# Kernel optimization log

Measured on AMD Instinct MI355X. Metric: run time of the kernel, lower is better.

The kernel has to match this reference:

```python
import jax, jax.numpy as jnp
import numpy as np

D = 256; H = 8; DH = D // H; FF = 1024; L = 2048; M = 1024


def _mlp(x, w0, b0, w1, b1, w2, b2):
    # 3-layer MLP, relu on all but last (matches MLP class)
    x = jax.nn.relu(x @ w0 + b0)
    x = jax.nn.relu(x @ w1 + b1)
    return x @ w2 + b2


def _ln(x, g, b, eps=1e-5):
    m = jnp.mean(x, axis=-1, keepdims=True)
    v = jnp.var(x, axis=-1, keepdims=True)
    return (x - m) * jax.lax.rsqrt(v + eps) * g + b


def setup_inputs():
    key = jax.random.key(0)
    ks = jax.random.split(key, 16)
    p = lambda i, shape: jax.random.normal(ks[i], shape, jnp.float32) * 0.02
    z = lambda *s: jnp.zeros(s, jnp.float32)
    o = lambda *s: jnp.ones(s, jnp.float32)
    # positions: ego covers [0, L), agent covers [L-M, 2L-M) -> exactly M shared positions
    return {
        'ego_q': jax.random.normal(ks[0], (1, L, D), jnp.float32),
        'agent_q': jax.random.normal(ks[1], (1, L, D), jnp.float32),
        'ego_pos': jnp.arange(L, dtype=jnp.int32),
        'agent_pos': jnp.arange(L, dtype=jnp.int32) + (L - M),
        'n_match': M,
        'fw0': p(2, (2 * D, D)), 'fb0': z(D),
        'fw1': p(3, (D, D)), 'fb1': z(D),
        'fw2': p(4, (D, D)), 'fb2': z(D),
        'wq': p(5, (D, D)), 'bq': z(D),
        'wk': p(6, (D, D)), 'bk': z(D),
        'wv': p(7, (D, D)), 'bv': z(D),
        'wo': p(8, (D, D)), 'bo': z(D),
        'g1': o(D), 'be1': z(D),
        'l1w': p(9, (D, FF)), 'l1b': z(FF),
        'l2w': p(10, (FF, D)), 'l2b': z(D),
        'g2': o(D), 'be2': z(D),
    }


def reference(ego_q, agent_q, ego_pos, agent_pos, n_match,
              fw0, fb0, fw1, fb1, fw2, fb2,
              wq, bq, wk, bk, wv, bv, wo, bo,
              g1, be1, l1w, l1b, l2w, l2b, g2, be2):
    La = agent_pos.shape[0]
    # vectorized replacement of the per-position dict/loop grouping:
    # for each ego position, find a matching agent position (positions sorted+unique)
    idx = jnp.clip(jnp.searchsorted(agent_pos, ego_pos), 0, La - 1)
    matched = (agent_pos[idx] == ego_pos)                     # (L,)
    pair = jnp.concatenate([ego_q, agent_q[:, idx, :]], axis=-1)  # (1, L, 2D)
    fused = _mlp(pair, fw0, fb0, fw1, fb1, fw2, fb2)          # (1, L, D)
    ego_out = jnp.where(matched[None, :, None], fused, ego_q)
    # agent queries whose positions are NOT in ego's set: indices [n_match, La)
    q = jnp.concatenate([ego_out, agent_q[:, n_match:, :]], axis=1)  # (1, 2L-M, D)
    kv = jnp.concatenate([ego_q, agent_q], axis=1)                   # (1, 2L, D)
    # MultiheadAttention (batch_first, eval mode -> no dropout)
    qh = (q @ wq + bq).reshape(1, -1, H, DH)
    kh = (kv @ wk + bk).reshape(1, -1, H, DH)
    vh = (kv @ wv + bv).reshape(1, -1, H, DH)
    scores = jnp.einsum('bqhd,bkhd->bhqk', qh, kh) * (1.0 / np.sqrt(DH))
    attn = jax.nn.softmax(scores, axis=-1)
    o = jnp.einsum('bhqk,bkhd->bqhd', attn, vh).reshape(1, -1, D) @ wo + bo
    x = _ln(q + o, g1, be1)
    ff = jax.nn.relu(x @ l1w + l1b) @ l2w + l2b
    return _ln(x + ff, g2, be2)
```

## Files before the change

### kernel.cpp

```cpp
#include <hip/hip_runtime.h>
#include <hip/hip_bf16.h>

typedef __hip_bfloat16 bf16;
typedef __bf16 bf16x8 __attribute__((ext_vector_type(8)));
typedef float  f32x16 __attribute__((ext_vector_type(16)));

__device__ __forceinline__ bool is_bf16_flag(const unsigned* g1w) {
    return *g1w == 0x3F803F80u;
}

__device__ __forceinline__ unsigned cvt_pk_bf16(float lo, float hi) {
    unsigned w;
    asm("v_cvt_pk_bf16_f32 %0, %1, %2" : "=v"(w) : "v"(lo), "v"(hi));
    return w;
}
__device__ __forceinline__ void permlane32_swap(unsigned& a, unsigned& b) {
    asm("v_permlane32_swap_b32 %0, %1" : "+v"(a), "+v"(b));
}

union FragU { unsigned u[4]; uint4 q; bf16x8 v; };

__device__ __forceinline__ float loadf(const void* p, size_t i, bool isb) {
    return isb ? __bfloat162float(((const bf16*)p)[i]) : ((const float*)p)[i];
}

__device__ __forceinline__ float4 load4rt(const void* p, size_t i, bool isb) {
    if (isb) {
        uint2 u = *(const uint2*)((const bf16*)p + i);
        float4 f;
        f.x = __uint_as_float(u.x << 16);
        f.y = __uint_as_float(u.x & 0xFFFF0000u);
        f.z = __uint_as_float(u.y << 16);
        f.w = __uint_as_float(u.y & 0xFFFF0000u);
        return f;
    }
    return *(const float4*)((const float*)p + i);
}

__device__ __forceinline__ void store4b(bf16* p, float4 v) {
    uint2 w;
    w.x = cvt_pk_bf16(v.x, v.y);
    w.y = cvt_pk_bf16(v.z, v.w);
    *(uint2*)p = w;
}

__device__ __forceinline__ float4 load4b(const bf16* p) {
    uint2 u = *(const uint2*)p;
    float4 f;
    f.x = __uint_as_float(u.x << 16);
    f.y = __uint_as_float(u.x & 0xFFFF0000u);
    f.z = __uint_as_float(u.y << 16);
    f.w = __uint_as_float(u.y & 0xFFFF0000u);
    return f;
}

#define NCVT 13
#define NWT 9
struct PreArgs {
    const void* csrc[NCVT];
    float*      cdst[NCVT];
    float       cscale[NCVT];
    int         cn4[NCVT];
    int         cblk_end[NCVT];
    int         cvt_blocks;
    const void* wsrc[NWT];
    bf16*       wdst[NWT];
    int         wK[NWT];
    int         wN[NWT];
    float       wscale[NWT];
    int         wblk_end[NWT];
    int         wt_blocks;
    const void* ego; const void* agent;
    const int*  epos; const int* apos;
    int         La; int L; int Mm;
    bf16*       pair;
    int*        mflag;
    int         pair_blocks;
    bf16*       kvb;
    int         kv_blocks;
    bf16*       qb;
};

__global__ void preprocess_kernel(PreArgs a, const unsigned* __restrict__ g1w) {
    bool isb = is_bf16_flag(g1w);
    __shared__ float ld[64][65];
    __shared__ int s_idx[2];
    int b = blockIdx.x;
    int tid = threadIdx.x;
    if (b < a.cvt_blocks) {
        int t = 0;
        while (b >= a.cblk_end[t]) t++;
        int base = (t == 0) ? 0 : a.cblk_end[t - 1];
        int i = (b - base) * 256 + tid;
        if (i >= a.cn4[t]) return;
        float sc = a.cscale[t];
        float4 r = load4rt(a.csrc[t], (size_t)i * 4, isb);
        r.x *= sc; r.y *= sc; r.z *= sc; r.w *= sc;
        ((float4*)a.cdst[t])[i] = r;
    } else if (b < a.cvt_blocks + a.wt_blocks) {
        b -= a.cvt_blocks;
        int w = 0;
        while (b >= a.wblk_end[w]) w++;
        int base = (w == 0) ? 0 : a.wblk_end[w - 1];
        int tt = b - base;
        int tn = a.wN[w] >> 6;
        int kr = (tt / tn) * 64, nc = (tt % tn) * 64;
        int N = a.wN[w], K = a.wK[w];
        float sc = a.wscale[w];
        const void* src = a.wsrc[w];
#pragma unroll
        for (int i = 0; i < 16; i++) {
            int f = tid + i * 256;
            int r = f >> 6, c = f & 63;
            ld[r][c] = loadf(src, (size_t)(kr + r) * N + nc + c, isb) * sc;
        }
        __syncthreads();
        bf16* dst = a.wdst[w];
#pragma unroll
        for (int i = 0; i < 16; i++) {
            int f = tid + i * 256;
            int c = f >> 6, r = f & 63;
            dst[(size_t)(nc + c) * K + kr + r] = __float2bfloat16(ld[r][c]);
        }
    } else if (b < a.cvt_blocks + a.wt_blocks + a.pair_blocks) {
        b -= a.cvt_blocks + a.wt_blocks;
        int rb = tid >> 7;
        int row = b * 2 + rb;
        int cc = (tid & 127) * 4;
        if ((tid & 127) == 0) {
            int p = a.epos[row];
            int lo = 0, hi = a.La;
            while (lo < hi) { int mid = (lo + hi) >> 1; if (a.apos[mid] < p) lo = mid + 1; else hi = mid; }
            int idx = lo < a.La - 1 ? lo : a.La - 1;
            s_idx[rb] = idx;
            a.mflag[row] = (a.apos[idx] == p) ? 1 : 0;
        }
        __syncthreads();
        int idx = s_idx[rb];
        float4 v = (cc < 256) ? load4rt(a.ego, (size_t)row * 256 + cc, isb)
                              : load4rt(a.agent, (size_t)idx * 256 + (cc - 256), isb);
        store4b(a.pair + (size_t)row * 512 + cc, v);
    } else if (b < a.cvt_blocks + a.wt_blocks + a.pair_blocks + a.kv_blocks) {
        b -= a.cvt_blocks + a.wt_blocks + a.pair_blocks;
        int wave = tid >> 6, lane = tid & 63;
        int r = b * 4 + wave;
        int col = lane * 4;
        float4 kvv = (r < a.L) ? load4rt(a.ego, (size_t)r * 256 + col, isb)
                               : load4rt(a.agent, (size_t)(r - a.L) * 256 + col, isb);
        store4b(a.kvb + (size_t)r * 256 + col, kvv);
    } else {
        b -= a.cvt_blocks + a.wt_blocks + a.pair_blocks + a.kv_blocks;
        int wave = tid >> 6, lane = tid & 63;
        int r = b * 4 + wave;
        int col = lane * 4;
        float4 qv = (r < a.L) ? load4rt(a.ego, (size_t)r * 256 + col, isb)
                              : load4rt(a.agent, (size_t)(a.Mm + r - a.L) * 256 + col, isb);
        store4b(a.qb + (size_t)r * 256 + col, qv);
    }
}

template<int RELU, int WMASK>
__device__ __forceinline__ void gemm_core(const bf16* __restrict__ A, const bf16* __restrict__ Bt,
                                          const float* __restrict__ bias, bf16* __restrict__ C,
                                          int K, int lda, int ldb, int ldc,
                                          int bm, int bn, bool addBias,
                                          const int* __restrict__ wmask,
                                          char* sA, char* sB) {
    const int t = threadIdx.x;
    const int lane = t & 63, wave = t >> 6;
    const int hi = lane >> 5, ql = lane & 31;
    const int wm = (wave & 1) * 32, wn = (wave >> 1) * 32;

    const int r0 = t >> 3, ch0 = t & 7;
    const int r1 = 32 + r0;
    const int wb0 = (r0 * 128 + ch0 * 16) ^ ((r0 & 7) << 4);
    const int wb1 = (r1 * 128 + ch0 * 16) ^ ((r1 & 7) << 4);

    uint4 ra0, ra1, rb0, rb1;
    ra0 = *(const uint4*)&A [(size_t)(bm + r0) * lda + ch0 * 8];
    ra1 = *(const uint4*)&A [(size_t)(bm + r1) * lda + ch0 * 8];
    rb0 = *(const uint4*)&Bt[(size_t)(bn + r0) * ldb + ch0 * 8];
    rb1 = *(const uint4*)&Bt[(size_t)(bn + r1) * ldb + ch0 * 8];

    f32x16 acc = {};
    const int swzA = ((wm + ql) & 7) << 4;
    const int swzB = ((wn + ql) & 7) << 4;
    const int rowA = (wm + ql) * 128;
    const int rowB = (wn + ql) * 128;

    for (int k0 = 0; k0 < K; k0 += 64) {
        __syncthreads();
        *(uint4*)(sA + wb0) = ra0;
        *(uint4*)(sA + wb1) = ra1;
        *(uint4*)(sB + wb0) = rb0;
        *(uint4*)(sB + wb1) = rb1;
        if (k0 + 64 < K) {
            int kn = k0 + 64;
            ra0 = *(const uint4*)&A [(size_t)(bm + r0) * lda + kn + ch0 * 8];
            ra1 = *(const uint4*)&A [(size_t)(bm + r1) * lda + kn + ch0 * 8];
            rb0 = *(const uint4*)&Bt[(size_t)(bn + r0) * ldb + kn + ch0 * 8];
            rb1 = *(const uint4*)&Bt[(size_t)(bn + r1) * ldb + kn + ch0 * 8];
        }
        __syncthreads();
#pragma unroll
        for (int kc = 0; kc < 4; kc++) {
            FragU af, bf_;
            af.q  = *(const uint4*)(sA + ((rowA + kc * 32 + hi * 16) ^ swzA));
            bf_.q = *(const uint4*)(sB + ((rowB + kc * 32 + hi * 16) ^ swzB));
            acc = __builtin_amdgcn_mfma_f32_32x32x16_bf16(af.v, bf_.v, acc, 0, 0, 0);
        }
    }

    int gn = bn + wn + ql;
    float bsv = addBias ? bias[gn] : 0.f;
#pragma unroll
    for (int r = 0; r < 16; r++) {
        int mrow = (r & 3) + 8 * (r >> 2) + 4 * hi;
        int grow = bm + wm + mrow;
        float v = acc[r] + bsv;
        if (RELU) v = fmaxf(v, 0.f);
        if (!WMASK || wmask[grow])
            C[(size_t)grow * ldc + gn] = __float2bfloat16(v);
    }
}

template<int RELU>
__launch_bounds__(256)
__global__ void gemm_bf16_kernel(const bf16* __restrict__ A, const bf16* __restrict__ Bt,
                                 const float* __restrict__ bias, bf16* __restrict__ C,
                                 int M, int N, int K, int lda, int ldb, int ldc) {
    __shared__ __align__(16) char sA[64 * 128];
    __shared__ __align__(16) char sB[64 * 128];
    const int z = blockIdx.z;
    gemm_core<RELU, 0>(A + (size_t)z * K, Bt + (size_t)z * K, bias, C + (size_t)z * M * ldc,
                       K, lda, ldb, ldc, blockIdx.y * 64, blockIdx.x * 64, z == 0, nullptr, sA, sB);
}

template<int RELU>
__launch_bounds__(256)
__global__ void gemm_masked_kernel(const bf16* __restrict__ A, const bf16* __restrict__ Bt,
                                   const float* __restrict__ bias, bf16* __restrict__ C,
                                   int K, int lda, int ldb, int ldc,
                                   const int* __restrict__ wmask) {
    __shared__ __align__(16) char sA[64 * 128];
    __shared__ __align__(16) char sB[64 * 128];
    gemm_core<RELU, 1>(A, Bt, bias, C, K, lda, ldb, ldc,
                       blockIdx.y * 64, blockIdx.x * 64, true, wmask, sA, sB);
}

struct GemmP {
    const bf16* A; const bf16* Bt; const float* bias; bf16* C;
    int K, lda, ldb, ldc, nx;
};

template<int R0, int R1>
__launch_bounds__(256)
__global__ void gemm_dual_kernel(GemmP p0, GemmP p1, int nblk0) {
    __shared__ __align__(16) char sA[64 * 128];
    __shared__ __align__(16) char sB[64 * 128];
    int b = blockIdx.x;
    if (b < nblk0) {
        int bn = (b % p0.nx) * 64, bm = (b / p0.nx) * 64;
        gemm_core<R0, 0>(p0.A, p0.Bt, p0.bias, p0.C, p0.K, p0.lda, p0.ldb, p0.ldc, bm, bn, true, nullptr, sA, sB);
    } else {
        b -= nblk0;
        int bn = (b % p1.nx) * 64, bm = (b / p1.nx) * 64;
        gemm_core<R1, 0>(p1.A, p1.Bt, p1.bias, p1.C, p1.K, p1.lda, p1.ldb, p1.ldc, bm, bn, true, nullptr, sA, sB);
    }
}

#define SPLITS 8

__launch_bounds__(256)
__global__ void attn_mfma_kernel(const bf16* __restrict__ qh,
                                 const bf16* __restrict__ kvh,
                                 float* __restrict__ pm, float* __restrict__ pl,
                                 bf16* __restrict__ pacc,
                                 int Nq, int Nk) {
    __shared__ __align__(16) char sK[2][64 * 128];
    __shared__ __align__(16) char sV[2][32 * 128];

    const int h = blockIdx.y, z = blockIdx.z;
    const int t = threadIdx.x;
    const int wave = t >> 6, lane = t & 63;
    const int ql = lane & 31, hi = lane >> 5;
    const int qbase = blockIdx.x * 128 + wave * 32;
    const int kbeg = z * (Nk / SPLITS);
    const int nkk = Nk / SPLITS;

    FragU qf0, qf1;
    {
        const bf16* qp = qh + (size_t)(qbase + ql) * 256 + h * 32;
        qf0.q = *(const uint4*)(qp + hi * 8);
        qf1.q = *(const uint4*)(qp + 16 + hi * 8);
    }

    float mrun = -1e30f, lrun = 0.f;
    f32x16 acc = {};

    const int skey = t >> 2, sch = t & 3;
    const int kwb = (skey * 128 + sch * 16) ^ ((skey & 7) << 4);

    uint4 rk = *(const uint4*)(kvh + (size_t)(kbeg + skey) * 512 + h * 32 + sch * 8);
    uint4 rv = *(const uint4*)(kvh + (size_t)(kbeg + lane) * 512 + 256 + h * 32 + wave * 8);

    int cur = 0;
#pragma unroll 1
    for (int t0 = 0; t0 < nkk; t0 += 64) {
        char* sKc = sK[cur];
        char* sVc = sV[cur];
        *(uint4*)(sKc + kwb) = rk;
        {
            unsigned short sv[8] = {
                (unsigned short)(rv.x), (unsigned short)(rv.x >> 16),
                (unsigned short)(rv.y), (unsigned short)(rv.y >> 16),
                (unsigned short)(rv.z), (unsigned short)(rv.z >> 16),
                (unsigned short)(rv.w), (unsigned short)(rv.w >> 16)};
#pragma unroll
            for (int i = 0; i < 8; i++) {
                int dh = wave * 8 + i;
                *(unsigned short*)(sVc + dh * 128 + ((lane * 2) ^ (i << 4))) = sv[i];
            }
        }
        if (t0 + 64 < nkk) {
            rk = *(const uint4*)(kvh + (size_t)(kbeg + t0 + 64 + skey) * 512 + h * 32 + sch * 8);
            rv = *(const uint4*)(kvh + (size_t)(kbeg + t0 + 64 + lane) * 512 + 256 + h * 32 + wave * 8);
        }
        __syncthreads();

        FragU ka, kb;
        f32x16 s0 = {}, s1 = {};
        {
            int row0 = ql, row1 = 32 + ql;
            int swzk = (ql & 7) << 4;
            ka.q = *(const uint4*)(sKc + ((row0 * 128 + hi * 16) ^ swzk));
            s0 = __builtin_amdgcn_mfma_f32_32x32x16_bf16(ka.v, qf0.v, s0, 0, 0, 0);
            ka.q = *(const uint4*)(sKc + ((row0 * 128 + 32 + hi * 16) ^ swzk));
            s0 = __builtin_amdgcn_mfma_f32_32x32x16_bf16(ka.v, qf1.v, s0, 0, 0, 0);
            kb.q = *(const uint4*)(sKc + ((row1 * 128 + hi * 16) ^ swzk));
            s1 = __builtin_amdgcn_mfma_f32_32x32x16_bf16(kb.v, qf0.v, s1, 0, 0, 0);
            kb.q = *(const uint4*)(sKc + ((row1 * 128 + 32 + hi * 16) ^ swzk));
            s1 = __builtin_amdgcn_mfma_f32_32x32x16_bf16(kb.v, qf1.v, s1, 0, 0, 0);
        }

        float tm = -1e30f;
#pragma unroll
        for (int r = 0; r < 16; r++) tm = fmaxf(tm, fmaxf(s0[r], s1[r]));
        tm = fmaxf(tm, __shfl_xor(tm, 32));
        if (!__all(tm <= mrun)) {
            float mn = fmaxf(mrun, tm);
            float cf = __builtin_amdgcn_exp2f(mrun - mn);
            mrun = mn;
#pragma unroll
            for (int r = 0; r < 16; r++) acc[r] *= cf;
            lrun *= cf;
        }

        float p0[16], p1[16];
        float ls = 0.f;
#pragma unroll
        for (int r = 0; r < 16; r++) { p0[r] = __builtin_amdgcn_exp2f(s0[r] - mrun); ls += p0[r]; }
#pragma unroll
        for (int r = 0; r < 16; r++) { p1[r] = __builtin_amdgcn_exp2f(s1[r] - mrun); ls += p1[r]; }
        ls += __shfl_xor(ls, 32);
        lrun += ls;

        int swzk = (ql & 7) << 4;
        FragU vf, pa;
        {
            unsigned a = cvt_pk_bf16(p0[0], p0[1]),  b = cvt_pk_bf16(p0[2], p0[3]);
            unsigned c = cvt_pk_bf16(p0[4], p0[5]),  d = cvt_pk_bf16(p0[6], p0[7]);
            permlane32_swap(a, c); permlane32_swap(b, d);
            pa.u[0] = a; pa.u[1] = b; pa.u[2] = c; pa.u[3] = d;
            vf.q = *(const uint4*)(sVc + ((ql * 128 + hi * 16) ^ swzk));
            acc = __builtin_amdgcn_mfma_f32_32x32x16_bf16(vf.v, pa.v, acc, 0, 0, 0);
            unsigned e = cvt_pk_bf16(p0[8], p0[9]),   f = cvt_pk_bf16(p0[10], p0[11]);
            unsigned g = cvt_pk_bf16(p0[12], p0[13]), h2 = cvt_pk_bf16(p0[14], p0[15]);
            permlane32_swap(e, g); permlane32_swap(f, h2);
            pa.u[0] = e; pa.u[1] = f; pa.u[2] = g; pa.u[3] = h2;
            vf.q = *(const uint4*)(sVc + ((ql * 128 + 32 + hi * 16) ^ swzk));
            acc = __builtin_amdgcn_mfma_f32_32x32x16_bf16(vf.v, pa.v, acc, 0, 0, 0);
        }
        {
            unsigned a = cvt_pk_bf16(p1[0], p1[1]),  b = cvt_pk_bf16(p1[2], p1[3]);
            unsigned c = cvt_pk_bf16(p1[4], p1[5]),  d = cvt_pk_bf16(p1[6], p1[7]);
            permlane32_swap(a, c); permlane32_swap(b, d);
            pa.u[0] = a; pa.u[1] = b; pa.u[2] = c; pa.u[3] = d;
            vf.q = *(const uint4*)(sVc + ((ql * 128 + 64 + hi * 16) ^ swzk));
            acc = __builtin_amdgcn_mfma_f32_32x32x16_bf16(vf.v, pa.v, acc, 0, 0, 0);
            unsigned e = cvt_pk_bf16(p1[8], p1[9]),   f = cvt_pk_bf16(p1[10], p1[11]);
            unsigned g = cvt_pk_bf16(p1[12], p1[13]), h2 = cvt_pk_bf16(p1[14], p1[15]);
            permlane32_swap(e, g); permlane32_swap(f, h2);
            pa.u[0] = e; pa.u[1] = f; pa.u[2] = g; pa.u[3] = h2;
            vf.q = *(const uint4*)(sVc + ((ql * 128 + 96 + hi * 16) ^ swzk));
            acc = __builtin_amdgcn_mfma_f32_32x32x16_bf16(vf.v, pa.v, acc, 0, 0, 0);
        }
        cur ^= 1;
    }

    if (hi == 0) {
        pm[((size_t)z * 8 + h) * Nq + qbase + ql] = mrun;
        pl[((size_t)z * 8 + h) * Nq + qbase + ql] = lrun;
    }
#pragma unroll
    for (int r = 0; r < 16; r++) {
        int dh = (r & 3) + 8 * (r >> 2) + 4 * hi;
        pacc[(((size_t)z * 8 + h) * 32 + dh) * (size_t)Nq + qbase + ql] = __float2bfloat16(acc[r]);
    }
}

__global__ void attn_merge_kernel(const float* __restrict__ pm, const float* __restrict__ pl,
                                  const bf16* __restrict__ pacc, bf16* __restrict__ o, int Nq) {
    int q = blockIdx.x * 256 + threadIdx.x;
    int h = blockIdx.y, dg = blockIdx.z;
    float ml[SPLITS];
    float M = -1e30f;
#pragma unroll
    for (int s = 0; s < SPLITS; s++) {
        ml[s] = pm[((size_t)s * 8 + h) * Nq + q];
        M = fmaxf(M, ml[s]);
    }
    float L = 0.f;
    float w[SPLITS];
#pragma unroll
    for (int s = 0; s < SPLITS; s++) {
        w[s] = __builtin_amdgcn_exp2f(ml[s] - M);
        L += pl[((size_t)s * 8 + h) * Nq + q] * w[s];
    }
    float inv = 1.f / L;
#pragma unroll
    for (int j = 0; j < 4; j++) {
        int d = dg * 4 + j;
        float a = 0.f;
#pragma unroll
        for (int s = 0; s < SPLITS; s++)
            a += __bfloat162float(pacc[(((size_t)s * 8 + h) * 32 + d) * (size_t)Nq + q]) * w[s];
        o[(size_t)q * 256 + h * 32 + d] = __float2bfloat16(a * inv);
    }
}

__global__ void ln_kernel(const bf16* __restrict__ a, const bf16* __restrict__ b,
                          const bf16* __restrict__ c,
                          const float* __restrict__ g, const float* __restrict__ be,
                          bf16* __restrict__ outf16, void* __restrict__ outb,
                          const unsigned* __restrict__ g1w) {
    int wave = threadIdx.x >> 6, lane = threadIdx.x & 63;
    int row = blockIdx.x * 4 + wave;
    int col = lane * 4;
    size_t base = (size_t)row * 256 + col;
    float4 av = load4b(a + base);
    float4 bv = load4b(b + base);
    float x0 = av.x + bv.x, x1 = av.y + bv.y, x2 = av.z + bv.z, x3 = av.w + bv.w;
    if (c) {
        float4 cv = load4b(c + base);
        x0 += cv.x; x1 += cv.y; x2 += cv.z; x3 += cv.w;
    }
    float s  = x0 + x1 + x2 + x3;
    float s2 = x0 * x0 + x1 * x1 + x2 * x2 + x3 * x3;
#pragma unroll
    for (int off = 32; off; off >>= 1) { s += __shfl_xor(s, off); s2 += __shfl_xor(s2, off); }
    float mean = s * (1.f / 256.f);
    float var  = s2 * (1.f / 256.f) - mean * mean;
    float rs = rsqrtf(var + 1e-5f);
    float4 gv = *(const float4*)(g + col);
    float4 bev = *(const float4*)(be + col);
    float y0 = (x0 - mean) * rs * gv.x + bev.x;
    float y1 = (x1 - mean) * rs * gv.y + bev.y;
    float y2 = (x2 - mean) * rs * gv.z + bev.z;
    float y3 = (x3 - mean) * rs * gv.w + bev.w;
    if (outf16) {
        store4b(outf16 + base, make_float4(y0, y1, y2, y3));
    } else if (is_bf16_flag(g1w)) {
        store4b((bf16*)outb + base, make_float4(y0, y1, y2, y3));
    } else {
        *(float4*)((float*)outb + base) = make_float4(y0, y1, y2, y3);
    }
}

extern "C" void kernel_launch(void* const* d_in, const int* in_sizes, int n_in,
                              void* d_out, int out_size, void* d_ws, size_t ws_size,
                              hipStream_t stream) {
    const int Dd = 256;
    const int L  = in_sizes[2];
    const int La = in_sizes[3];
    const int Nk = L + La;
    const int Nq = out_size / Dd;
    const int Mm = L + La - Nq;
    const float scale = 0.17677669529663687f * 1.4426950408889634f;

    const unsigned* g1w = (const unsigned*)d_in[19];

    float* W = (float*)d_ws;
    size_t off = 0;
    auto alloc = [&](size_t n) { size_t o = off; off += n; return o; };
    (void)ws_size; (void)n_in;

    size_t o_fb0 = alloc(256), o_fb1 = alloc(256), o_fb2 = alloc(256);
    size_t o_bq = alloc(256), o_bkv = alloc(512), o_bo = alloc(256);
    size_t o_g1 = alloc(256), o_be1 = alloc(256);
    size_t o_l1b = alloc(1024), o_l2b = alloc(256);
    size_t o_g2 = alloc(256), o_be2 = alloc(256);

    size_t o_fw0t = alloc(65536), o_fw1t = alloc(32768), o_fw2t = alloc(32768);
    size_t o_wqt = alloc(32768), o_wkvt = alloc(65536), o_wot = alloc(32768);
    size_t o_l1wt = alloc(131072), o_l2wt = alloc(131072);
    size_t o_pair = alloc((size_t)L * 256);
    size_t o_h1 = alloc((size_t)L * 128), o_h2 = alloc((size_t)L * 128);
    size_t o_q   = alloc((size_t)Nq * 128);
    size_t o_kv  = alloc((size_t)Nk * 128);
    size_t o_qh  = alloc((size_t)Nq * 128);
    size_t o_kvh = alloc((size_t)Nk * 256);
    size_t o_ao  = alloc((size_t)Nq * 128);
    size_t o_opp = alloc((size_t)Nq * 256);
    size_t o_x   = alloc((size_t)Nq * 128);
    size_t o_ff1 = alloc((size_t)Nq * 512);
    size_t o_ff2p = alloc((size_t)Nq * 256);
    size_t o_pacc = alloc((size_t)SPLITS * 8 * 16 * Nq);
    size_t o_pm   = alloc((size_t)SPLITS * 8 * Nq);
    size_t o_pl   = alloc((size_t)SPLITS * 8 * Nq);
    size_t o_ints = alloc((size_t)L);
    int* mflag = (int*)(W + o_ints);

    auto B16 = [&](size_t o) { return (bf16*)(W + o); };

    {
        PreArgs pa;
        const int csrcs[NCVT] = {6, 8, 10, 12, 14, 16, 18, 19, 20, 22, 24, 25, 26};
        const size_t cdsts[NCVT] = {o_fb0, o_fb1, o_fb2, o_bq, o_bkv, o_bkv + 256, o_bo,
                                    o_g1, o_be1, o_l1b, o_l2b, o_g2, o_be2};
        int blk = 0;
        for (int i = 0; i < NCVT; i++) {
            pa.csrc[i] = d_in[csrcs[i]];
            pa.cdst[i] = W + cdsts[i];
            pa.cscale[i] = (csrcs[i] == 12) ? scale : 1.0f;
            pa.cn4[i] = in_sizes[csrcs[i]] / 4;
            blk += (pa.cn4[i] + 255) / 256;
            pa.cblk_end[i] = blk;
        }
        pa.cvt_blocks = blk;

        const int wsrcs[NWT] = {5, 7, 9, 11, 13, 15, 17, 21, 23};
        bf16* wdsts[NWT] = {B16(o_fw0t), B16(o_fw1t), B16(o_fw2t), B16(o_wqt),
                            B16(o_wkvt), B16(o_wkvt) + 65536, B16(o_wot),
                            B16(o_l1wt), B16(o_l2wt)};
        const int Ks[NWT] = {512, 256, 256, 256, 256, 256, 256, 256, 1024};
        const int Ns[NWT] = {256, 256, 256, 256, 256, 256, 256, 1024, 256};
        int wblk = 0;
        for (int i = 0; i < NWT; i++) {
            pa.wsrc[i] = d_in[wsrcs[i]];
            pa.wdst[i] = wdsts[i];
            pa.wK[i] = Ks[i]; pa.wN[i] = Ns[i];
            pa.wscale[i] = (wsrcs[i] == 11) ? scale : 1.0f;
            wblk += (Ks[i] / 64) * (Ns[i] / 64);
            pa.wblk_end[i] = wblk;
        }
        pa.wt_blocks = wblk;

        pa.ego = d_in[0]; pa.agent = d_in[1];
        pa.epos = (const int*)d_in[2]; pa.apos = (const int*)d_in[3];
        pa.La = La; pa.L = L; pa.Mm = Mm;
        pa.pair = B16(o_pair); pa.mflag = mflag;
        pa.pair_blocks = L / 2;
        pa.kvb = B16(o_kv);
        pa.kv_blocks = Nk / 4;
        pa.qb = B16(o_q);

        int total = pa.cvt_blocks + pa.wt_blocks + pa.pair_blocks + pa.kv_blocks + Nq / 4;
        preprocess_kernel<<<total, 256, 0, stream>>>(pa, g1w);
    }

    {
        GemmP p0{B16(o_pair), B16(o_fw0t), W + o_fb0, B16(o_h1),  512, 512, 512, 256, 4};
        GemmP p1{B16(o_kv),   B16(o_wkvt), W + o_bkv, B16(o_kvh), 256, 256, 256, 512, 8};
        int nblk0 = 4 * (L / 64);
        int nblk1 = 8 * (Nk / 64);
        gemm_dual_kernel<1, 0><<<nblk0 + nblk1, 256, 0, stream>>>(p0, p1, nblk0);
    }

    gemm_bf16_kernel<1><<<dim3(4, L/64), 256, 0, stream>>>(B16(o_h1), B16(o_fw1t), W + o_fb1, B16(o_h2), L, 256, 256, 256, 256, 256);
    gemm_masked_kernel<0><<<dim3(4, L/64), 256, 0, stream>>>(B16(o_h2), B16(o_fw2t), W + o_fb2, B16(o_q), 256, 256, 256, 256, mflag);

    gemm_bf16_kernel<0><<<dim3(4, Nq/64), 256, 0, stream>>>(B16(o_q), B16(o_wqt), W + o_bq, B16(o_qh), Nq, 256, 256, 256, 256, 256);

    attn_mfma_kernel<<<dim3(Nq/128, 8, SPLITS), 256, 0, stream>>>(B16(o_qh), B16(o_kvh),
                                                                  W + o_pm, W + o_pl, B16(o_pacc),
                                                                  Nq, Nk);
    attn_merge_kernel<<<dim3(Nq/256, 8, 8), 256, 0, stream>>>(W + o_pm, W + o_pl, B16(o_pacc),
                                                              B16(o_ao), Nq);

    gemm_bf16_kernel<0><<<dim3(4, Nq/64, 2), 256, 0, stream>>>(B16(o_ao), B16(o_wot), W + o_bo, B16(o_opp), Nq, 256, 128, 256, 256, 256);
    ln_kernel<<<Nq / 4, 256, 0, stream>>>(B16(o_q), B16(o_opp), B16(o_opp) + (size_t)Nq * 256,
                                          W + o_g1, W + o_be1, B16(o_x), nullptr, g1w);

    gemm_bf16_kernel<1><<<dim3(16, Nq/64), 256, 0, stream>>>(B16(o_x),   B16(o_l1wt), W + o_l1b, B16(o_ff1), Nq, 1024, 256, 256, 256, 1024);
    gemm_bf16_kernel<0><<<dim3(4,  Nq/64, 2), 256, 0, stream>>>(B16(o_ff1), B16(o_l2wt), W + o_l2b, B16(o_ff2p), Nq, 256, 512, 1024, 1024, 256);
    ln_kernel<<<Nq / 4, 256, 0, stream>>>(B16(o_x), B16(o_ff2p), B16(o_ff2p) + (size_t)Nq * 256,
                                          W + o_g2, W + o_be2, nullptr, d_out, g1w);
}
```

Baseline: 95.05 us.

## Write V projection transposed so attention loads V with vector stores

The fused K/V projection is split into separate K and V GEMMs. The V GEMM writes its output transposed, staging it through shared memory so the global stores stay coalesced. The attention kernel can then load V tiles with one 16-byte LDS store instead of eight scalar scattered stores per thread. The weight-transpose preprocessing is also vectorised to use float4 loads and 4-wide bf16 stores. These changes add an extra shared-memory round trip and two barriers in the V GEMM epilogue.

```diff
diff --git a/kernel.cpp b/kernel.cpp
--- a/kernel.cpp
+++ b/kernel.cpp
@@ -109,18 +109,25 @@
         float sc = a.wscale[w];
         const void* src = a.wsrc[w];
 #pragma unroll
-        for (int i = 0; i < 16; i++) {
-            int f = tid + i * 256;
-            int r = f >> 6, c = f & 63;
-            ld[r][c] = loadf(src, (size_t)(kr + r) * N + nc + c, isb) * sc;
+        for (int i = 0; i < 4; i++) {
+            int idx4 = tid + i * 256;
+            int r = idx4 >> 4;
+            int c4 = (idx4 & 15) * 4;
+            float4 v = load4rt(src, (size_t)(kr + r) * N + nc + c4, isb);
+            ld[r][c4]     = v.x * sc;
+            ld[r][c4 + 1] = v.y * sc;
+            ld[r][c4 + 2] = v.z * sc;
+            ld[r][c4 + 3] = v.w * sc;
         }
         __syncthreads();
         bf16* dst = a.wdst[w];
 #pragma unroll
-        for (int i = 0; i < 16; i++) {
-            int f = tid + i * 256;
-            int c = f >> 6, r = f & 63;
-            dst[(size_t)(nc + c) * K + kr + r] = __float2bfloat16(ld[r][c]);
+        for (int i = 0; i < 4; i++) {
+            int idx4 = tid + i * 256;
+            int c = idx4 >> 4;
+            int r4 = (idx4 & 15) * 4;
+            float4 v = make_float4(ld[r4][c], ld[r4 + 1][c], ld[r4 + 2][c], ld[r4 + 3][c]);
+            store4b(dst + (size_t)(nc + c) * K + kr + r4, v);
         }
     } else if (b < a.cvt_blocks + a.wt_blocks + a.pair_blocks) {
         b -= a.cvt_blocks + a.wt_blocks;
@@ -159,7 +166,7 @@
     }
 }
 
-template<int RELU, int WMASK>
+template<int RELU, int WMASK, int VT>
 __device__ __forceinline__ void gemm_core(const bf16* __restrict__ A, const bf16* __restrict__ Bt,
                                           const float* __restrict__ bias, bf16* __restrict__ C,
                                           int K, int lda, int ldb, int ldc,
@@ -213,6 +220,26 @@
 
     int gn = bn + wn + ql;
     float bsv = addBias ? bias[gn] : 0.f;
+    if (VT) {
+        __syncthreads();
+        int gnl = wn + ql;
+#pragma unroll
+        for (int r = 0; r < 16; r++) {
+            int mrow = (r & 3) + 8 * (r >> 2) + 4 * hi;
+            int keyl = wm + mrow;
+            float v = acc[r] + bsv;
+            *(bf16*)(sA + gnl * 128 + ((keyl * 2) ^ ((gnl & 7) << 4))) = __float2bfloat16(v);
+        }
+        __syncthreads();
+        int row = t >> 2, quad = t & 3;
+#pragma unroll
+        for (int cc = 0; cc < 2; cc++) {
+            int chunk = quad * 2 + cc;
+            uint4 v = *(const uint4*)(sA + row * 128 + ((chunk * 16) ^ ((row & 7) << 4)));
+            *(uint4*)(C + (size_t)(bn + row) * ldc + bm + chunk * 8) = v;
+        }
+        return;
+    }
 #pragma unroll
     for (int r = 0; r < 16; r++) {
         int mrow = (r & 3) + 8 * (r >> 2) + 4 * hi;
@@ -232,8 +259,8 @@
     __shared__ __align__(16) char sA[64 * 128];
     __shared__ __align__(16) char sB[64 * 128];
     const int z = blockIdx.z;
-    gemm_core<RELU, 0>(A + (size_t)z * K, Bt + (size_t)z * K, bias, C + (size_t)z * M * ldc,
-                       K, lda, ldb, ldc, blockIdx.y * 64, blockIdx.x * 64, z == 0, nullptr, sA, sB);
+    gemm_core<RELU, 0, 0>(A + (size_t)z * K, Bt + (size_t)z * K, bias, C + (size_t)z * M * ldc,
+                          K, lda, ldb, ldc, blockIdx.y * 64, blockIdx.x * 64, z == 0, nullptr, sA, sB);
 }
 
 template<int RELU>
@@ -244,8 +271,8 @@
                                    const int* __restrict__ wmask) {
     __shared__ __align__(16) char sA[64 * 128];
     __shared__ __align__(16) char sB[64 * 128];
-    gemm_core<RELU, 1>(A, Bt, bias, C, K, lda, ldb, ldc,
-                       blockIdx.y * 64, blockIdx.x * 64, true, wmask, sA, sB);
+    gemm_core<RELU, 1, 0>(A, Bt, bias, C, K, lda, ldb, ldc,
+                          blockIdx.y * 64, blockIdx.x * 64, true, wmask, sA, sB);
 }
 
 struct GemmP {
@@ -255,17 +282,21 @@
 
 template<int R0, int R1>
 __launch_bounds__(256)
-__global__ void gemm_dual_kernel(GemmP p0, GemmP p1, int nblk0) {
+__global__ void gemm_triple_kernel(GemmP p0, GemmP p1, GemmP p2, int nblk0, int nblk1) {
     __shared__ __align__(16) char sA[64 * 128];
     __shared__ __align__(16) char sB[64 * 128];
     int b = blockIdx.x;
     if (b < nblk0) {
         int bn = (b % p0.nx) * 64, bm = (b / p0.nx) * 64;
-        gemm_core<R0, 0>(p0.A, p0.Bt, p0.bias, p0.C, p0.K, p0.lda, p0.ldb, p0.ldc, bm, bn, true, nullptr, sA, sB);
-    } else {
+        gemm_core<R0, 0, 0>(p0.A, p0.Bt, p0.bias, p0.C, p0.K, p0.lda, p0.ldb, p0.ldc, bm, bn, true, nullptr, sA, sB);
+    } else if (b < nblk0 + nblk1) {
         b -= nblk0;
         int bn = (b % p1.nx) * 64, bm = (b / p1.nx) * 64;
-        gemm_core<R1, 0>(p1.A, p1.Bt, p1.bias, p1.C, p1.K, p1.lda, p1.ldb, p1.ldc, bm, bn, true, nullptr, sA, sB);
+        gemm_core<R1, 0, 0>(p1.A, p1.Bt, p1.bias, p1.C, p1.K, p1.lda, p1.ldb, p1.ldc, bm, bn, true, nullptr, sA, sB);
+    } else {
+        b -= nblk0 + nblk1;
+        int bn = (b % p2.nx) * 64, bm = (b / p2.nx) * 64;
+        gemm_core<0, 0, 1>(p2.A, p2.Bt, p2.bias, p2.C, p2.K, p2.lda, p2.ldb, p2.ldc, bm, bn, true, nullptr, sA, sB);
     }
 }
 
@@ -273,7 +304,8 @@
 
 __launch_bounds__(256)
 __global__ void attn_mfma_kernel(const bf16* __restrict__ qh,
-                                 const bf16* __restrict__ kvh,
+                                 const bf16* __restrict__ kh,
+                                 const bf16* __restrict__ vt,
                                  float* __restrict__ pm, float* __restrict__ pl,
                                  bf16* __restrict__ pacc,
                                  int Nq, int Nk) {
@@ -300,9 +332,12 @@
 
     const int skey = t >> 2, sch = t & 3;
     const int kwb = (skey * 128 + sch * 16) ^ ((skey & 7) << 4);
-
-    uint4 rk = *(const uint4*)(kvh + (size_t)(kbeg + skey) * 512 + h * 32 + sch * 8);
-    uint4 rv = *(const uint4*)(kvh + (size_t)(kbeg + lane) * 512 + 256 + h * 32 + wave * 8);
+    const int vrow = t >> 3, vch = t & 7;
+    const int vwb = (vrow * 128 + vch * 16) ^ ((vrow & 7) << 4);
+    const bf16* vbase = vt + (size_t)(h * 32 + vrow) * Nk;
+
+    uint4 rk = *(const uint4*)(kh + (size_t)(kbeg + skey) * 256 + h * 32 + sch * 8);
+    uint4 rv = *(const uint4*)(vbase + kbeg + vch * 8);
 
     int cur = 0;
 #pragma unroll 1
@@ -310,21 +345,10 @@
         char* sKc = sK[cur];
         char* sVc = sV[cur];
         *(uint4*)(sKc + kwb) = rk;
-        {
-            unsigned short sv[8] = {
-                (unsigned short)(rv.x), (unsigned short)(rv.x >> 16),
-                (unsigned short)(rv.y), (unsigned short)(rv.y >> 16),
-                (unsigned short)(rv.z), (unsigned short)(rv.z >> 16),
-                (unsigned short)(rv.w), (unsigned short)(rv.w >> 16)};
-#pragma unroll
-            for (int i = 0; i < 8; i++) {
-                int dh = wave * 8 + i;
-                *(unsigned short*)(sVc + dh * 128 + ((lane * 2) ^ (i << 4))) = sv[i];
-            }
-        }
+        *(uint4*)(sVc + vwb) = rv;
         if (t0 + 64 < nkk) {
-            rk = *(const uint4*)(kvh + (size_t)(kbeg + t0 + 64 + skey) * 512 + h * 32 + sch * 8);
-            rv = *(const uint4*)(kvh + (size_t)(kbeg + t0 + 64 + lane) * 512 + 256 + h * 32 + wave * 8);
+            rk = *(const uint4*)(kh + (size_t)(kbeg + t0 + 64 + skey) * 256 + h * 32 + sch * 8);
+            rv = *(const uint4*)(vbase + kbeg + t0 + 64 + vch * 8);
         }
         __syncthreads();
 
@@ -509,7 +533,8 @@
     size_t o_q   = alloc((size_t)Nq * 128);
     size_t o_kv  = alloc((size_t)Nk * 128);
     size_t o_qh  = alloc((size_t)Nq * 128);
-    size_t o_kvh = alloc((size_t)Nk * 256);
+    size_t o_kh  = alloc((size_t)Nk * 128);
+    size_t o_vt  = alloc((size_t)Nk * 128);
     size_t o_ao  = alloc((size_t)Nq * 128);
     size_t o_opp = alloc((size_t)Nq * 256);
     size_t o_x   = alloc((size_t)Nq * 128);
@@ -570,11 +595,13 @@
     }
 
     {
-        GemmP p0{B16(o_pair), B16(o_fw0t), W + o_fb0, B16(o_h1),  512, 512, 512, 256, 4};
-        GemmP p1{B16(o_kv),   B16(o_wkvt), W + o_bkv, B16(o_kvh), 256, 256, 256, 512, 8};
+        GemmP p0{B16(o_pair), B16(o_fw0t), W + o_fb0, B16(o_h1), 512, 512, 512, 256, 4};
+        GemmP p1{B16(o_kv), B16(o_wkvt), W + o_bkv, B16(o_kh), 256, 256, 256, 256, 4};
+        GemmP p2{B16(o_kv), B16(o_wkvt) + 65536, W + o_bkv + 256, B16(o_vt), 256, 256, 256, Nk, 4};
         int nblk0 = 4 * (L / 64);
-        int nblk1 = 8 * (Nk / 64);
-        gemm_dual_kernel<1, 0><<<nblk0 + nblk1, 256, 0, stream>>>(p0, p1, nblk0);
+        int nblk1 = 4 * (Nk / 64);
+        int nblk2 = 4 * (Nk / 64);
+        gemm_triple_kernel<1, 0><<<nblk0 + nblk1 + nblk2, 256, 0, stream>>>(p0, p1, p2, nblk0, nblk1);
     }
 
     gemm_bf16_kernel<1><<<dim3(4, L/64), 256, 0, stream>>>(B16(o_h1), B16(o_fw1t), W + o_fb1, B16(o_h2), L, 256, 256, 256, 256, 256);
@@ -582,7 +609,7 @@
 
     gemm_bf16_kernel<0><<<dim3(4, Nq/64), 256, 0, stream>>>(B16(o_q), B16(o_wqt), W + o_bq, B16(o_qh), Nq, 256, 256, 256, 256, 256);
 
-    attn_mfma_kernel<<<dim3(Nq/128, 8, SPLITS), 256, 0, stream>>>(B16(o_qh), B16(o_kvh),
+    attn_mfma_kernel<<<dim3(Nq/128, 8, SPLITS), 256, 0, stream>>>(B16(o_qh), B16(o_kh), B16(o_vt),
                                                                   W + o_pm, W + o_pl, B16(o_pacc),
                                                                   Nq, Nk);
     attn_merge_kernel<<<dim3(Nq/256, 8, 8), 256, 0, stream>>>(W + o_pm, W + o_pl, B16(o_pacc),
```

New measurement: 91.29 us, median of 2. 3.9% less time.
